# Kernel tuning notes

Measured on AMD Instinct MI355X. Metric: run time of the kernel, lower is better.

Reference implementation:

```python
import jax, jax.numpy as jnp
import numpy as np

B, S, D, DFF = 4, 2048, 1024, 4096
EPS = 1e-5


def layernorm(x, gamma, beta):
    mu = jnp.mean(x, axis=-1, keepdims=True)
    var = jnp.var(x, axis=-1, keepdims=True)
    return (x - mu) * jax.lax.rsqrt(var + EPS) * gamma + beta


def attention(Q, K, V, causal):
    d_k = Q.shape[-1]
    scores = jnp.einsum('bqd,bkd->bqk', Q, K) / jnp.sqrt(jnp.asarray(d_k, Q.dtype))
    if causal:
        q_len, k_len = scores.shape[-2], scores.shape[-1]
        mask = jnp.tril(jnp.ones((q_len, k_len), dtype=bool))
        scores = jnp.where(mask[None], scores, jnp.asarray(-jnp.inf, scores.dtype))
    w = jax.nn.softmax(scores, axis=-1)
    return jnp.einsum('bqk,bkd->bqd', w, V)


def setup_inputs() -> dict:
    key = jax.random.key(0)
    ks = jax.random.split(key, 12)
    sd = 0.02
    return {
        'y': jax.random.normal(ks[0], (B, S, D), jnp.float32),
        'Z': jax.random.normal(ks[1], (B, S, D), jnp.float32),
        'w1': jax.random.normal(ks[2], (D, DFF), jnp.float32) * sd,
        'b1': jnp.zeros((DFF,), jnp.float32),
        'w2': jax.random.normal(ks[3], (DFF, D), jnp.float32) * sd,
        'b2': jnp.zeros((D,), jnp.float32),
        'g1': jnp.ones((D,), jnp.float32), 'beta1': jnp.zeros((D,), jnp.float32),
        'g2': jnp.ones((D,), jnp.float32), 'beta2': jnp.zeros((D,), jnp.float32),
        'g3': jnp.ones((D,), jnp.float32), 'beta3': jnp.zeros((D,), jnp.float32),
    }


def reference(y, Z, w1, b1, w2, b2, g1, beta1, g2, beta2, g3, beta3):
    # masked (causal) self-attention, single head over full d_model
    sa = attention(y, y, y, causal=True)
    y = layernorm(y + sa, g1, beta1)
    # cross-attention to encoder memory Z
    ca = attention(y, Z, Z, causal=False)
    y = layernorm(y + ca, g2, beta2)
    # position-wise FFN
    h = jax.nn.relu(jnp.einsum('bsd,df->bsf', y, w1) + b1)
    ff = jnp.einsum('bsf,fd->bsd', h, w2) + b2
    y = layernorm(y + ff, g3, beta3)
    return y
```

## Files before the change

### kernel.cpp

```cpp
#include <hip/hip_runtime.h>
#include <hip/hip_bf16.h>
#include <hip/hip_fp8.h>


#define Bb 4
#define Ss 2048
#define Dd 1024
#define Ff 4096

typedef __attribute__((ext_vector_type(4))) float f32x4;
typedef __attribute__((ext_vector_type(8))) short bf16x8;
typedef __attribute__((ext_vector_type(2))) long i64x2;
typedef __attribute__((ext_vector_type(8))) unsigned short u16x8;
typedef __attribute__((ext_vector_type(4))) unsigned short u16x4;

__device__ __forceinline__ unsigned short f2bf(float f) {
  unsigned u = __float_as_uint(f);
  u += 0x7FFFu + ((u >> 16) & 1u);
  return (unsigned short)(u >> 16);
}
__device__ __forceinline__ float bf2f(unsigned short h) {
  return __uint_as_float(((unsigned)h) << 16);
}
__device__ __forceinline__ unsigned char f2f8(float f) {
  __hip_fp8_e4m3 q(f);
  return q.__x;
}
__device__ __forceinline__ int f8col(int c) {
  int g = c >> 6, b = c & 63, o = b >> 3, j = b & 7;
  return g * 64 + (2 * (o & 3) + (o >> 2)) * 8 + j;
}

__device__ __forceinline__ void gload_lds16(const void* g, void* l) {
  __builtin_amdgcn_global_load_lds((const __attribute__((address_space(1))) void*)g,
                                   (__attribute__((address_space(3))) void*)l, 16, 0, 0);
}

__device__ __forceinline__ int xcd8(int orig, int n) {
  int q = n >> 3, r = n & 7;
  int x = orig & 7;
  int base = x < r ? x * (q + 1) : r * (q + 1) + (x - r) * q;
  return base + (orig >> 3);
}

__global__ __launch_bounds__(256) void k_transpose_cast(const float* __restrict__ in,
                                                        unsigned short* __restrict__ outT,
                                                        unsigned char* __restrict__ out8,
                                                        int R, int C) {
  __shared__ float t[32][33];
  size_t bo = (size_t)blockIdx.z * R * C;
  const float* pin = in + bo;
  unsigned short* poutT = outT + bo;
  unsigned char* pout8 = out8 ? out8 + bo : nullptr;
  int c0 = blockIdx.x * 32, r0 = blockIdx.y * 32;
  int tx = threadIdx.x, ty = threadIdx.y;
#pragma unroll
  for (int i = 0; i < 4; i++) {
    float v = pin[(size_t)(r0 + ty + i * 8) * C + c0 + tx];
    t[ty + i * 8][tx] = v;
    if (pout8) pout8[(size_t)(r0 + ty + i * 8) * C + f8col(c0 + tx)] = f2f8(v);
  }
  __syncthreads();
#pragma unroll
  for (int i = 0; i < 4; i++)
    poutT[(size_t)(c0 + ty + i * 8) * R + r0 + tx] = f2bf(t[tx][ty + i * 8]);
}

#define BAR() __builtin_amdgcn_s_barrier()
#define PRIO1() __builtin_amdgcn_s_setprio(1)
#define PRIO0() __builtin_amdgcn_s_setprio(0)

#define LDA8(arr, mh, bo)                                                       \
  {                                                                             \
    _Pragma("unroll") for (int j_ = 0; j_ < QM; ++j_) {                         \
      _Pragma("unroll") for (int kh_ = 0; kh_ < 2; ++kh_) {                     \
        arr[j_][kh_] =                                                          \
            *(const bf16x8*)(lds + (bo) + ((mh)*QM + j_) * 2048 + aof[kh_]);    \
      }                                                                         \
    }                                                                           \
  }

#define LDB8(arr, nh, bo)                                                       \
  {                                                                             \
    _Pragma("unroll") for (int n_ = 0; n_ < 2; ++n_) {                          \
      _Pragma("unroll") for (int kh_ = 0; kh_ < 2; ++kh_) {                     \
        arr[n_][kh_] =                                                          \
            *(const bf16x8*)(lds + (bo) + ((nh)*2 + n_) * 2048 + bof[kh_]);     \
      }                                                                         \
    }                                                                           \
  }

#define MMQ(aarr, barr, mh, nh)                                                 \
  {                                                                             \
    _Pragma("unroll") for (int j_ = 0; j_ < QM; ++j_) {                         \
      _Pragma("unroll") for (int n_ = 0; n_ < 2; ++n_) {                        \
        _Pragma("unroll") for (int kh_ = 0; kh_ < 2; ++kh_) {                   \
          acc[(mh)*QM + j_][(nh)*2 + n_] = __builtin_amdgcn_mfma_f32_16x16x32_bf16( \
              aarr[j_][kh_], barr[n_][kh_], acc[(mh)*QM + j_][(nh)*2 + n_], 0, 0, 0); \
        }                                                                       \
      }                                                                         \
    }                                                                           \
  }

#define LDAF8(arr, mh, bo)                                                      \
  {                                                                             \
    _Pragma("unroll") for (int j_ = 0; j_ < 4; ++j_)                            \
        arr[j_] = *(const i64x2*)(lds + (bo) + ((mh)*4 + j_) * 1024 + aofs);    \
  }
#define LDBF8(arr, nh, bo)                                                      \
  {                                                                             \
    _Pragma("unroll") for (int n_ = 0; n_ < 2; ++n_)                            \
        arr[n_] = *(const i64x2*)(lds + (bo) + ((nh)*2 + n_) * 1024 + bofs);    \
  }
#define MMQF8(aarr, barr, mh, nh)                                               \
  {                                                                             \
    _Pragma("unroll") for (int j_ = 0; j_ < 4; ++j_) {                          \
      _Pragma("unroll") for (int n_ = 0; n_ < 2; ++n_) {                        \
        _Pragma("unroll") for (int kh_ = 0; kh_ < 2; ++kh_) {                   \
          acc[(mh)*4 + j_][(nh)*2 + n_] = __builtin_amdgcn_mfma_f32_16x16x32_fp8_fp8( \
              aarr[j_][kh_], barr[n_][kh_], acc[(mh)*4 + j_][(nh)*2 + n_], 0, 0, 0);  \
        }                                                                       \
      }                                                                         \
    }                                                                           \
  }

#define EPILOGUE(MR_, WMS_)                                                     \
  {                                                                             \
    const int colb = j0 + wc * 64 + fr;                                         \
    const int rowb = i0 + wr * (WMS_) + (kq << 2);                              \
    const size_t cb = (size_t)bz * bsC;                                         \
    _Pragma("unroll") for (int m = 0; m < (MR_); ++m) {                         \
      _Pragma("unroll") for (int r = 0; r < 4; ++r) {                           \
        size_t ro = cb + (size_t)(rowb + m * 16 + r) * ldc;                     \
        _Pragma("unroll") for (int n = 0; n < 4; ++n) {                         \
          float v = acc[m][n][r];                                               \
          int col = colb + n * 16;                                              \
          if (EPI == 0) Cb[ro + col] = f2bf(v * scale);                         \
          else if (EPI == 2) Cb[ro + col] = f2bf(fmaxf(v + bias[col], 0.f));    \
          else if (EPI == 4) Cb[ro + col] = f2bf(v + residF[ro + col]);         \
          else if (EPI == 6) Cb[ro + col] = f2bf(v + bf2f(residB[ro + col]));   \
          else Cb[ro + col] = f2bf(v + bias[col] + bf2f(residB[ro + col]));     \
        }                                                                       \
      }                                                                         \
    }                                                                           \
  }

template <bool CAUSAL>
__global__ __launch_bounds__(512) void k_gemm8f8(
    const unsigned char* __restrict__ Ag, const unsigned char* __restrict__ Bg,
    unsigned short* __restrict__ Cb,
    int K, int lda, int ldb, int ldc, long bsA, long bsB, long bsC, float scale) {
  constexpr int ABYTES = 16384, BBYTES = 16384;
  __shared__ alignas(16) char lds[2 * ABYTES + 2 * BBYTES];

  int i0, j0;
  if (CAUSAL) {
    int t = xcd8(blockIdx.x, gridDim.x);
    int ti = (int)((sqrtf(8.f * t + 1.f) - 1.f) * 0.5f);
    while ((ti + 1) * (ti + 2) / 2 <= t) ++ti;
    while (ti * (ti + 1) / 2 > t) --ti;
    i0 = ti * 256;
    j0 = (t - ti * (ti + 1) / 2) * 256;
  } else {
    int lin = xcd8(blockIdx.y * gridDim.x + blockIdx.x, gridDim.x * gridDim.y);
    i0 = (lin / gridDim.x) * 256;
    j0 = (lin % gridDim.x) * 256;
  }
  int bz = blockIdx.z;
  Ag += (size_t)bz * bsA;
  Bg += (size_t)bz * bsB;

  const int nk = K / 64;
  const int niter = nk / 2;

  const int tid = threadIdx.x;
  const int w = tid >> 6, lane = tid & 63;
  const int wr = w >> 2, wc = w & 3;

  const int srow = tid >> 2;
  const int scs = (tid & 3) ^ ((tid >> 3) & 3);
  const unsigned char* As = Ag + (size_t)(i0 + srow) * lda + scs * 16;
  const unsigned char* Bs = Bg + (size_t)(j0 + srow) * ldb + scs * 16;

  auto stA = [&](int kt, int hf) {
    int ks = kt < nk ? kt : nk - 1;
    gload_lds16(As + (size_t)(hf * 128) * lda + ks * 64,
                lds + (kt & 1) * ABYTES + hf * 8192 + w * 1024);
  };
  auto stB = [&](int kt, int hf) {
    int ks = kt < nk ? kt : nk - 1;
    gload_lds16(Bs + (size_t)(hf * 128) * ldb + ks * 64,
                lds + 2 * ABYTES + (kt & 1) * BBYTES + hf * 8192 + w * 1024);
  };

  const int fr = lane & 15, kq = lane >> 4;
  const int rA = wr * 128 + fr;
  const int rB = wc * 64 + fr;
  const unsigned aofs = rA * 64 + ((kq ^ ((rA >> 1) & 3)) << 4);
  const unsigned bofs = rB * 64 + ((kq ^ ((rB >> 1) & 3)) << 4);
  constexpr int A0 = 0, A1 = ABYTES, B0 = 2 * ABYTES, B1 = 2 * ABYTES + BBYTES;

  f32x4 acc[8][4];
#pragma unroll
  for (int m = 0; m < 8; ++m)
#pragma unroll
    for (int n = 0; n < 4; ++n) acc[m][n] = (f32x4){0.f, 0.f, 0.f, 0.f};

  i64x2 a0[4], a1[4], b0[2], b1[2];

  stA(0, 0); stA(0, 1); stB(0, 0); stB(0, 1);
  stA(1, 0); stA(1, 1); stB(1, 0);
  asm volatile("s_waitcnt vmcnt(3)" ::: "memory");
  BAR();
  LDAF8(a0, 0, A0); LDBF8(b0, 0, B0);

  for (int t = 0; t < niter; ++t) {
    const int ka = 2 * t + 2, kb = 2 * t + 3;
    LDAF8(a1, 1, A0);
    stB(2 * t + 1, 1);
    BAR(); PRIO1(); MMQF8(a0, b0, 0, 0); PRIO0(); BAR();
    LDBF8(b1, 1, B0);
    stA(ka, 0);
    BAR(); PRIO1(); MMQF8(a1, b0, 1, 0); PRIO0(); BAR();
    stA(ka, 1);
    BAR(); PRIO1(); MMQF8(a0, b1, 0, 1); PRIO0(); BAR();
    stB(ka, 0);
    asm volatile("s_waitcnt vmcnt(3)" ::: "memory");
    BAR();
    LDAF8(a0, 0, A1); LDBF8(b0, 0, B1);
    PRIO1(); MMQF8(a1, b1, 1, 1); PRIO0(); BAR();
    LDAF8(a1, 1, A1);
    stB(ka, 1);
    BAR(); PRIO1(); MMQF8(a0, b0, 0, 0); PRIO0(); BAR();
    LDBF8(b1, 1, B1);
    stA(kb, 0);
    BAR(); PRIO1(); MMQF8(a1, b0, 1, 0); PRIO0(); BAR();
    stA(kb, 1);
    BAR(); PRIO1(); MMQF8(a0, b1, 0, 1); PRIO0(); BAR();
    stB(kb, 0);
    asm volatile("s_waitcnt vmcnt(3)" ::: "memory");
    BAR();
    LDAF8(a0, 0, A0); LDBF8(b0, 0, B0);
    PRIO1(); MMQF8(a1, b1, 1, 1); PRIO0(); BAR();
  }

  const int colb = j0 + wc * 64 + fr;
  const int rowb = i0 + wr * 128 + (kq << 2);
  const size_t cb = (size_t)bz * bsC;
#pragma unroll
  for (int m = 0; m < 8; ++m) {
#pragma unroll
    for (int r = 0; r < 4; ++r) {
      size_t ro = cb + (size_t)(rowb + m * 16 + r) * ldc;
#pragma unroll
      for (int n = 0; n < 4; ++n)
        Cb[ro + colb + n * 16] = f2bf(acc[m][n][r] * scale);
    }
  }
}

template <int EPI, bool CAUSAL>
__global__ __launch_bounds__(512) void k_gemm8(
    const unsigned short* __restrict__ Ag, const unsigned short* __restrict__ Bg,
    unsigned short* __restrict__ Cb,
    const float* __restrict__ bias, const float* __restrict__ residF,
    const unsigned short* __restrict__ residB,
    int K, int lda, int ldb, int ldc, long bsA, long bsB, long bsC, float scale) {
  constexpr int QM = 4;
  constexpr int ABYTES = 32768, BBYTES = 32768;
  __shared__ alignas(16) char lds[2 * ABYTES + 2 * BBYTES];

  int i0, j0;
  if (CAUSAL) {
    int t = xcd8(blockIdx.x, gridDim.x);
    int ti = (int)((sqrtf(8.f * t + 1.f) - 1.f) * 0.5f);
    while ((ti + 1) * (ti + 2) / 2 <= t) ++ti;
    while (ti * (ti + 1) / 2 > t) --ti;
    i0 = ti * 256;
    j0 = (t - ti * (ti + 1) / 2) * 256;
  } else {
    int lin = xcd8(blockIdx.y * gridDim.x + blockIdx.x, gridDim.x * gridDim.y);
    i0 = (lin / gridDim.x) * 256;
    j0 = (lin % gridDim.x) * 256;
  }
  int bz = blockIdx.z;
  Ag += (size_t)bz * bsA;
  Bg += (size_t)bz * bsB;

  const int nk = K / 64;
  const int niter = nk / 2;

  const int tid = threadIdx.x;
  const int w = tid >> 6, lane = tid & 63;
  const int wr = w >> 2, wc = w & 3;

  const int srow = (w << 3) + (lane >> 3);
  const int bcs = (lane & 7) ^ (lane >> 3);
  const unsigned short* As = Ag + (size_t)(i0 + srow) * lda + bcs * 8;
  const unsigned short* Bs = Bg + (size_t)(j0 + srow) * ldb + bcs * 8;
  char* ldsAw = lds + w * 1024;
  char* ldsBw = lds + 2 * ABYTES + w * 1024;

  auto stA = [&](int kt, int hf) {
    int ks = kt < nk ? kt : nk - 1;
#pragma unroll
    for (int l = 0; l < 2; ++l)
      gload_lds16(As + (size_t)(hf * 128 + l * 64) * lda + ks * 64,
                  ldsAw + (kt & 1) * ABYTES + hf * 128 * 128 + l * 8192);
  };
  auto stB = [&](int kt, int hf) {
    int ks = kt < nk ? kt : nk - 1;
#pragma unroll
    for (int l = 0; l < 2; ++l)
      gload_lds16(Bs + (size_t)(hf * 128 + l * 64) * ldb + ks * 64,
                  ldsBw + (kt & 1) * BBYTES + hf * 128 * 128 + l * 8192);
  };

  const int fr = lane & 15, kq = lane >> 4;
  const int rA = wr * 128 + fr;
  const int rB = wc * 64 + fr;
  unsigned aof[2], bof[2];
  aof[0] = rA * 128 + ((kq ^ (rA & 7)) << 4);
  aof[1] = rA * 128 + (((kq + 4) ^ (rA & 7)) << 4);
  bof[0] = 2 * ABYTES + rB * 128 + ((kq ^ (rB & 7)) << 4);
  bof[1] = 2 * ABYTES + rB * 128 + (((kq + 4) ^ (rB & 7)) << 4);
  constexpr int A0 = 0, A1 = ABYTES, B0 = 0, B1 = BBYTES;

  f32x4 acc[8][4];
#pragma unroll
  for (int m = 0; m < 8; ++m)
#pragma unroll
    for (int n = 0; n < 4; ++n) acc[m][n] = (f32x4){0.f, 0.f, 0.f, 0.f};

  bf16x8 a0[QM][2], a1[QM][2], b0[2][2], b1[2][2];

  stA(0, 0); stA(0, 1); stB(0, 0); stB(0, 1);
  stA(1, 0); stA(1, 1); stB(1, 0);
  asm volatile("s_waitcnt vmcnt(6)" ::: "memory");
  BAR();
  LDA8(a0, 0, A0); LDB8(b0, 0, B0);

  for (int t = 0; t < niter; ++t) {
    const int ka = 2 * t + 2, kb = 2 * t + 3;
    LDA8(a1, 1, A0);
    stB(2 * t + 1, 1);
    BAR(); PRIO1(); MMQ(a0, b0, 0, 0); PRIO0(); BAR();
    LDB8(b1, 1, B0);
    stA(ka, 0);
    BAR(); PRIO1(); MMQ(a1, b0, 1, 0); PRIO0(); BAR();
    stA(ka, 1);
    BAR(); PRIO1(); MMQ(a0, b1, 0, 1); PRIO0(); BAR();
    stB(ka, 0);
    asm volatile("s_waitcnt vmcnt(6)" ::: "memory");
    BAR();
    LDA8(a0, 0, A1); LDB8(b0, 0, B1);
    PRIO1(); MMQ(a1, b1, 1, 1); PRIO0(); BAR();
    LDA8(a1, 1, A1);
    stB(ka, 1);
    BAR(); PRIO1(); MMQ(a0, b0, 0, 0); PRIO0(); BAR();
    LDB8(b1, 1, B1);
    stA(kb, 0);
    BAR(); PRIO1(); MMQ(a1, b0, 1, 0); PRIO0(); BAR();
    stA(kb, 1);
    BAR(); PRIO1(); MMQ(a0, b1, 0, 1); PRIO0(); BAR();
    stB(kb, 0);
    asm volatile("s_waitcnt vmcnt(6)" ::: "memory");
    BAR();
    LDA8(a0, 0, A0); LDB8(b0, 0, B0);
    PRIO1(); MMQ(a1, b1, 1, 1); PRIO0(); BAR();
  }
  EPILOGUE(8, 128)
}

template <int EPI, bool KCAP>
__global__ __launch_bounds__(512) void k_gemm4(
    const unsigned short* __restrict__ Ag, const unsigned short* __restrict__ Bg,
    unsigned short* __restrict__ Cb,
    const float* __restrict__ bias, const float* __restrict__ residF,
    const unsigned short* __restrict__ residB,
    int K, int lda, int ldb, int ldc, long bsA, long bsB, long bsC, float scale) {
  constexpr int QM = 4;
  constexpr int ABYTES = 16384, BBYTES = 32768;
  __shared__ alignas(16) char lds[2 * ABYTES + 2 * BBYTES];

  int lin = xcd8(blockIdx.y * gridDim.x + blockIdx.x, gridDim.x * gridDim.y);
  int i0 = (lin / gridDim.x) * 128;
  int j0 = (lin % gridDim.x) * 256;
  int bz = blockIdx.z;
  Ag += (size_t)bz * bsA;
  Bg += (size_t)bz * bsB;

  int nk = K / 64;
  if (KCAP) {
    int cap = i0 / 64 + 2;
    nk = nk < cap ? nk : cap;
  }
  const int niter = nk / 2;

  const int tid = threadIdx.x;
  const int w = tid >> 6, lane = tid & 63;
  const int wr = w >> 2, wc = w & 3;

  const int srow = (w << 3) + (lane >> 3);
  const int bcs = (lane & 7) ^ (lane >> 3);
  const unsigned short* As = Ag + (size_t)(i0 + srow) * lda + bcs * 8;
  const unsigned short* Bs = Bg + (size_t)(j0 + srow) * ldb + bcs * 8;
  char* ldsAw = lds + w * 1024;
  char* ldsBw = lds + 2 * ABYTES + w * 1024;

  auto stA2 = [&](int kt) {
    int ks = kt < nk ? kt : nk - 1;
#pragma unroll
    for (int hf = 0; hf < 2; ++hf)
      gload_lds16(As + (size_t)(hf * 64) * lda + ks * 64,
                  ldsAw + (kt & 1) * ABYTES + hf * 64 * 128);
  };
  auto stBh = [&](int kt, int hf) {
    int ks = kt < nk ? kt : nk - 1;
#pragma unroll
    for (int l = 0; l < 2; ++l)
      gload_lds16(Bs + (size_t)(hf * 128 + l * 64) * ldb + ks * 64,
                  ldsBw + (kt & 1) * BBYTES + hf * 128 * 128 + l * 8192);
  };

  const int fr = lane & 15, kq = lane >> 4;
  const int rA = wr * 64 + fr;
  const int rB = wc * 64 + fr;
  unsigned aof[2], bof[2];
  aof[0] = rA * 128 + ((kq ^ (rA & 7)) << 4);
  aof[1] = rA * 128 + (((kq + 4) ^ (rA & 7)) << 4);
  bof[0] = 2 * ABYTES + rB * 128 + ((kq ^ (rB & 7)) << 4);
  bof[1] = 2 * ABYTES + rB * 128 + (((kq + 4) ^ (rB & 7)) << 4);
  constexpr int A0 = 0, A1 = ABYTES, B0 = 0, B1 = BBYTES;

  f32x4 acc[4][4];
#pragma unroll
  for (int m = 0; m < 4; ++m)
#pragma unroll
    for (int n = 0; n < 4; ++n) acc[m][n] = (f32x4){0.f, 0.f, 0.f, 0.f};

  bf16x8 a[QM][2], b0[2][2], b1[2][2];

  stA2(0); stBh(0, 0); stBh(0, 1);
  stA2(1); stBh(1, 0);
  asm volatile("s_waitcnt vmcnt(4)" ::: "memory");
  BAR();
  LDA8(a, 0, A0); LDB8(b0, 0, B0);

  for (int t = 0; t < niter; ++t) {
    const int ka = 2 * t + 2, kb = 2 * t + 3;
    LDB8(b1, 1, B0);
    stBh(2 * t + 1, 1);
    BAR(); PRIO1(); MMQ(a, b0, 0, 0); PRIO0(); BAR();
    stA2(ka); stBh(ka, 0);
    asm volatile("s_waitcnt vmcnt(4)" ::: "memory");
    BAR();
    PRIO1(); MMQ(a, b1, 0, 1); PRIO0();
    LDA8(a, 0, A1); LDB8(b0, 0, B1);
    BAR();
    LDB8(b1, 1, B1);
    stBh(ka, 1);
    BAR(); PRIO1(); MMQ(a, b0, 0, 0); PRIO0(); BAR();
    stA2(kb); stBh(kb, 0);
    asm volatile("s_waitcnt vmcnt(4)" ::: "memory");
    BAR();
    PRIO1(); MMQ(a, b1, 0, 1); PRIO0();
    LDA8(a, 0, A0); LDB8(b0, 0, B0);
    BAR();
  }
  EPILOGUE(4, 64)
}

template <bool CAUSAL>
__global__ __launch_bounds__(256) void k_softmax(unsigned short* __restrict__ scores) {
  int row = blockIdx.x;
  int i = row & (Ss - 1);
  unsigned short* src = scores + (size_t)row * Ss;
  int nv = CAUSAL ? i + 1 : Ss;
  int nb = CAUSAL ? ((i & ~127) + 128) : Ss;
  int t = threadIdx.x;
  int w = t >> 6, lane = t & 63;
  bool act = t * 8 < nb;
  float v[8];
  float mx = -1e30f;
  if (act) {
    u16x8 raw = *(const u16x8*)(src + t * 8);
#pragma unroll
    for (int k = 0; k < 8; k++) {
      int j = t * 8 + k;
      v[k] = (j < nv) ? bf2f(raw[k]) : -1e30f;
      mx = fmaxf(mx, v[k]);
    }
  } else {
#pragma unroll
    for (int k = 0; k < 8; k++) v[k] = -1e30f;
  }
#pragma unroll
  for (int o = 32; o; o >>= 1) mx = fmaxf(mx, __shfl_xor(mx, o));
  __shared__ float red[8];
  if (lane == 0) red[w] = mx;
  __syncthreads();
  mx = fmaxf(fmaxf(red[0], red[1]), fmaxf(red[2], red[3]));
  float sum = 0.f;
#pragma unroll
  for (int k = 0; k < 8; k++) {
    float e = (v[k] > -1e29f) ? __expf(v[k] - mx) : 0.f;
    v[k] = e;
    sum += e;
  }
#pragma unroll
  for (int o = 32; o; o >>= 1) sum += __shfl_xor(sum, o);
  if (lane == 0) red[4 + w] = sum;
  __syncthreads();
  sum = red[4] + red[5] + red[6] + red[7];
  float inv = 1.f / sum;
  if (act) {
    u16x8 r;
#pragma unroll
    for (int k = 0; k < 8; k++) r[k] = f2bf(v[k] * inv);
    *(u16x8*)(src + t * 8) = r;
  }
}

template <int OM>
__global__ __launch_bounds__(256) void k_ln(const unsigned short* __restrict__ a,
                                            const float* __restrict__ g,
                                            const float* __restrict__ be,
                                            float* __restrict__ outf,
                                            unsigned short* __restrict__ outb,
                                            unsigned char* __restrict__ out8) {
  int row = blockIdx.x;
  size_t o = (size_t)row * Dd;
  int t = threadIdx.x;
  u16x4 raw = *(const u16x4*)(a + o + t * 4);
  f32x4 x;
#pragma unroll
  for (int k = 0; k < 4; k++) x[k] = bf2f(raw[k]);
  float s = x[0] + x[1] + x[2] + x[3];
  float q = x[0] * x[0] + x[1] * x[1] + x[2] * x[2] + x[3] * x[3];
  int w = t >> 6, lane = t & 63;
#pragma unroll
  for (int of = 32; of; of >>= 1) {
    s += __shfl_xor(s, of);
    q += __shfl_xor(q, of);
  }
  __shared__ float red[8];
  if (lane == 0) {
    red[w] = s;
    red[4 + w] = q;
  }
  __syncthreads();
  s = red[0] + red[1] + red[2] + red[3];
  q = red[4] + red[5] + red[6] + red[7];
  float mean = s * (1.f / Dd);
  float var = q * (1.f / Dd) - mean * mean;
  float rstd = rsqrtf(var + 1e-5f);
  f32x4 gv = *(const f32x4*)(g + t * 4);
  f32x4 bv = *(const f32x4*)(be + t * 4);
  f32x4 y;
#pragma unroll
  for (int k = 0; k < 4; k++) y[k] = (x[k] - mean) * rstd * gv[k] + bv[k];
  if (OM == 0) {
    *(f32x4*)(outf + o + t * 4) = y;
  } else {
    u16x4 r;
    r[0] = f2bf(y[0]); r[1] = f2bf(y[1]); r[2] = f2bf(y[2]); r[3] = f2bf(y[3]);
    *(u16x4*)(outb + o + t * 4) = r;
    if (OM == 2) {
      int cbyte = t * 4;
      int gq = cbyte >> 6, oo = (cbyte >> 3) & 7, j = cbyte & 7;
      int phys = gq * 64 + (2 * (oo & 3) + (oo >> 2)) * 8 + j;
      unsigned rr = (unsigned)f2f8(y[0]) | ((unsigned)f2f8(y[1]) << 8) |
                    ((unsigned)f2f8(y[2]) << 16) | ((unsigned)f2f8(y[3]) << 24);
      *(unsigned*)(out8 + (size_t)row * Dd + phys) = rr;
    }
  }
}

extern "C" void kernel_launch(void* const* d_in, const int* in_sizes, int n_in, void* d_out,
                              int out_size, void* d_ws, size_t ws_size, hipStream_t stream) {
  (void)in_sizes; (void)n_in; (void)out_size; (void)ws_size;
  const float* y   = (const float*)d_in[0];
  const float* Z   = (const float*)d_in[1];
  const float* w1  = (const float*)d_in[2];
  const float* b1  = (const float*)d_in[3];
  const float* w2  = (const float*)d_in[4];
  const float* b2  = (const float*)d_in[5];
  const float* g1  = (const float*)d_in[6];
  const float* be1 = (const float*)d_in[7];
  const float* g2  = (const float*)d_in[8];
  const float* be2 = (const float*)d_in[9];
  const float* g3  = (const float*)d_in[10];
  const float* be3 = (const float*)d_in[11];
  float* out = (float*)d_out;

  char* ws = (char*)d_ws;
  const size_t MB = 1024ull * 1024ull;
  unsigned short* T   = (unsigned short*)(ws);
  unsigned short* y1b = (unsigned short*)(ws);
  unsigned short* ffo = (unsigned short*)(ws);
  unsigned short* Zt  = (unsigned short*)(ws + 16 * MB);
  unsigned short* ybf = (unsigned short*)(ws + 32 * MB);
  unsigned short* w1t = (unsigned short*)(ws + 48 * MB);
  unsigned short* w2t = (unsigned short*)(ws + 56 * MB);
  unsigned short* sc  = (unsigned short*)(ws + 64 * MB);
  unsigned short* h   = (unsigned short*)(ws + 64 * MB);
  unsigned char* y8   = (unsigned char*)(ws + 96 * MB);
  unsigned char* Z8   = (unsigned char*)(ws + 104 * MB);
  unsigned char* y18  = (unsigned char*)(ws + 112 * MB);
  unsigned short* attnb = (unsigned short*)d_out;

  dim3 b256(256), b512(512);
  const float scl = 1.f / 32.f;
  const long SD = (long)Ss * Dd, SS = (long)Ss * Ss;

  k_transpose_cast<<<dim3(Dd / 32, Ss / 32, Bb), dim3(32, 8), 0, stream>>>(y, T, y8, Ss, Dd);
  k_transpose_cast<<<dim3(Dd / 32, Ss / 32, Bb), dim3(32, 8), 0, stream>>>(Z, Zt, Z8, Ss, Dd);
  k_transpose_cast<<<dim3(Ff / 32, Dd / 32, 1), dim3(32, 8), 0, stream>>>(w1, w1t, nullptr, Dd, Ff);
  k_transpose_cast<<<dim3(Dd / 32, Ff / 32, 1), dim3(32, 8), 0, stream>>>(w2, w2t, nullptr, Ff, Dd);

  k_gemm8f8<true><<<dim3(36, 1, Bb), b512, 0, stream>>>(
      y8, y8, sc, Dd, Dd, Dd, Ss, SD, SD, SS, scl);
  k_softmax<true><<<dim3(Bb * Ss), b256, 0, stream>>>(sc);
  k_gemm4<4, true><<<dim3(Dd / 256, Ss / 128, Bb), b512, 0, stream>>>(
      sc, T, attnb, nullptr, y, nullptr, Ss, Ss, Ss, Dd, SS, SD, SD, 1.f);
  k_ln<2><<<dim3(Bb * Ss), b256, 0, stream>>>(attnb, g1, be1, nullptr, y1b, y18);

  k_gemm8f8<false><<<dim3(Ss / 256, Ss / 256, Bb), b512, 0, stream>>>(
      y18, Z8, sc, Dd, Dd, Dd, Ss, SD, SD, SS, scl);
  k_softmax<false><<<dim3(Bb * Ss), b256, 0, stream>>>(sc);
  k_gemm4<6, false><<<dim3(Dd / 256, Ss / 128, Bb), b512, 0, stream>>>(
      sc, Zt, attnb, nullptr, nullptr, y1b, Ss, Ss, Ss, Dd, SS, SD, SD, 1.f);
  k_ln<1><<<dim3(Bb * Ss), b256, 0, stream>>>(attnb, g2, be2, nullptr, ybf, nullptr);

  k_gemm8<2, false><<<dim3(Ff / 256, (Bb * Ss) / 256, 1), b512, 0, stream>>>(
      ybf, w1t, h, b1, nullptr, nullptr, Dd, Dd, Dd, Ff, 0L, 0L, 0L, 1.f);
  k_gemm4<7, false><<<dim3(Dd / 256, (Bb * Ss) / 128, 1), b512, 0, stream>>>(
      h, w2t, ffo, b2, nullptr, ybf, Ff, Ff, Ff, Dd, 0L, 0L, 0L, 1.f);
  k_ln<0><<<dim3(Bb * Ss), b256, 0, stream>>>(ffo, g3, be3, out, nullptr, nullptr);
}
```

Before: 353.5 us.

## Split causal PV GEMM over K into two halves, sum partials in layernorm

Replaces the causal P·V GEMM with a dedicated kernel that splits each row-tile's causal K range into two balanced halves run by separate blocks. Each half writes a bf16 partial, the first including the fp32 residual, and the following layernorm adds the two partials. This doubles the grid and evens out the triangular work so the GPU is better filled. It also merges the y and Z transpose/cast launches into one. The cost is an extra bf16 partial buffer written and read, plus partial sums rounded to bf16 before they are added.

```diff
diff --git a/kernel.cpp b/kernel.cpp
--- a/kernel.cpp
+++ b/kernel.cpp
@@ -43,23 +43,46 @@
   return base + (orig >> 3);
 }
 
-__global__ __launch_bounds__(256) void k_transpose_cast(const float* __restrict__ in,
-                                                        unsigned short* __restrict__ outT,
-                                                        unsigned char* __restrict__ out8,
-                                                        int R, int C) {
+__global__ __launch_bounds__(256) void k_transpose2(const float* __restrict__ inA,
+                                                    const float* __restrict__ inB,
+                                                    unsigned short* __restrict__ outTA,
+                                                    unsigned short* __restrict__ outTB,
+                                                    unsigned char* __restrict__ out8A,
+                                                    unsigned char* __restrict__ out8B,
+                                                    int R, int C) {
   __shared__ float t[32][33];
-  size_t bo = (size_t)blockIdx.z * R * C;
-  const float* pin = in + bo;
-  unsigned short* poutT = outT + bo;
-  unsigned char* pout8 = out8 ? out8 + bo : nullptr;
+  int z = blockIdx.z;
+  bool second = z >= Bb;
+  int b = second ? z - Bb : z;
+  size_t bo = (size_t)b * R * C;
+  const float* pin = (second ? inB : inA) + bo;
+  unsigned short* poutT = (second ? outTB : outTA) + bo;
+  unsigned char* pout8 = (second ? out8B : out8A) + bo;
   int c0 = blockIdx.x * 32, r0 = blockIdx.y * 32;
   int tx = threadIdx.x, ty = threadIdx.y;
 #pragma unroll
   for (int i = 0; i < 4; i++) {
     float v = pin[(size_t)(r0 + ty + i * 8) * C + c0 + tx];
     t[ty + i * 8][tx] = v;
-    if (pout8) pout8[(size_t)(r0 + ty + i * 8) * C + f8col(c0 + tx)] = f2f8(v);
-  }
+    pout8[(size_t)(r0 + ty + i * 8) * C + f8col(c0 + tx)] = f2f8(v);
+  }
+  __syncthreads();
+#pragma unroll
+  for (int i = 0; i < 4; i++)
+    poutT[(size_t)(c0 + ty + i * 8) * R + r0 + tx] = f2bf(t[tx][ty + i * 8]);
+}
+
+__global__ __launch_bounds__(256) void k_transpose_cast(const float* __restrict__ in,
+                                                        unsigned short* __restrict__ outT,
+                                                        int R, int C) {
+  __shared__ float t[32][33];
+  const float* pin = in;
+  unsigned short* poutT = outT;
+  int c0 = blockIdx.x * 32, r0 = blockIdx.y * 32;
+  int tx = threadIdx.x, ty = threadIdx.y;
+#pragma unroll
+  for (int i = 0; i < 4; i++)
+    t[ty + i * 8][tx] = pin[(size_t)(r0 + ty + i * 8) * C + c0 + tx];
   __syncthreads();
 #pragma unroll
   for (int i = 0; i < 4; i++)
@@ -137,7 +160,6 @@
           int col = colb + n * 16;                                              \
           if (EPI == 0) Cb[ro + col] = f2bf(v * scale);                         \
           else if (EPI == 2) Cb[ro + col] = f2bf(fmaxf(v + bias[col], 0.f));    \
-          else if (EPI == 4) Cb[ro + col] = f2bf(v + residF[ro + col]);         \
           else if (EPI == 6) Cb[ro + col] = f2bf(v + bf2f(residB[ro + col]));   \
           else Cb[ro + col] = f2bf(v + bias[col] + bf2f(residB[ro + col]));     \
         }                                                                       \
@@ -263,8 +285,7 @@
 __global__ __launch_bounds__(512) void k_gemm8(
     const unsigned short* __restrict__ Ag, const unsigned short* __restrict__ Bg,
     unsigned short* __restrict__ Cb,
-    const float* __restrict__ bias, const float* __restrict__ residF,
-    const unsigned short* __restrict__ residB,
+    const float* __restrict__ bias, const unsigned short* __restrict__ residB,
     int K, int lda, int ldb, int ldc, long bsA, long bsB, long bsC, float scale) {
   constexpr int QM = 4;
   constexpr int ABYTES = 32768, BBYTES = 32768;
@@ -376,8 +397,7 @@
 __global__ __launch_bounds__(512) void k_gemm4(
     const unsigned short* __restrict__ Ag, const unsigned short* __restrict__ Bg,
     unsigned short* __restrict__ Cb,
-    const float* __restrict__ bias, const float* __restrict__ residF,
-    const unsigned short* __restrict__ residB,
+    const float* __restrict__ bias, const unsigned short* __restrict__ residB,
     int K, int lda, int ldb, int ldc, long bsA, long bsB, long bsC, float scale) {
   constexpr int QM = 4;
   constexpr int ABYTES = 16384, BBYTES = 32768;
@@ -469,6 +489,120 @@
     BAR();
   }
   EPILOGUE(4, 64)
+}
+
+__global__ __launch_bounds__(512) void k_pv1(
+    const unsigned short* __restrict__ Ag, const unsigned short* __restrict__ Bg,
+    unsigned short* __restrict__ C0, unsigned short* __restrict__ C1,
+    const float* __restrict__ residF) {
+  constexpr int QM = 4;
+  constexpr int ABYTES = 16384, BBYTES = 32768;
+  __shared__ alignas(16) char lds[2 * ABYTES + 2 * BBYTES];
+  const int lda = Ss, ldb = Ss, ldc = Dd;
+
+  const int xc = blockIdx.x & 3, kh = blockIdx.x >> 2;
+  const int iy = blockIdx.y;
+  const int i0 = iy * 128, j0 = xc * 256;
+  const int bz = blockIdx.z;
+  Ag += (size_t)bz * ((long)Ss * Ss);
+  Bg += (size_t)bz * ((long)Dd * Ss);
+
+  const int cap = 2 * iy + 2;
+  const int nA = (iy + 2) & ~1;
+  const int kbase = kh ? nA : 0;
+  const int nkr = kh ? cap - nA : nA;
+  const int niter = nkr / 2;
+
+  const int tid = threadIdx.x;
+  const int w = tid >> 6, lane = tid & 63;
+  const int wr = w >> 2, wc = w & 3;
+
+  const int srow = (w << 3) + (lane >> 3);
+  const int bcs = (lane & 7) ^ (lane >> 3);
+  const unsigned short* As = Ag + (size_t)(i0 + srow) * lda + bcs * 8;
+  const unsigned short* Bs = Bg + (size_t)(j0 + srow) * ldb + bcs * 8;
+  char* ldsAw = lds + w * 1024;
+  char* ldsBw = lds + 2 * ABYTES + w * 1024;
+
+  auto stA2 = [&](int kt) {
+    int ks = kbase + (kt < nkr ? kt : (nkr > 0 ? nkr - 1 : 0));
+#pragma unroll
+    for (int hf = 0; hf < 2; ++hf)
+      gload_lds16(As + (size_t)(hf * 64) * lda + ks * 64,
+                  ldsAw + (kt & 1) * ABYTES + hf * 64 * 128);
+  };
+  auto stBh = [&](int kt, int hf) {
+    int ks = kbase + (kt < nkr ? kt : (nkr > 0 ? nkr - 1 : 0));
+#pragma unroll
+    for (int l = 0; l < 2; ++l)
+      gload_lds16(Bs + (size_t)(hf * 128 + l * 64) * ldb + ks * 64,
+                  ldsBw + (kt & 1) * BBYTES + hf * 128 * 128 + l * 8192);
+  };
+
+  const int fr = lane & 15, kq = lane >> 4;
+  const int rA = wr * 64 + fr;
+  const int rB = wc * 64 + fr;
+  unsigned aof[2], bof[2];
+  aof[0] = rA * 128 + ((kq ^ (rA & 7)) << 4);
+  aof[1] = rA * 128 + (((kq + 4) ^ (rA & 7)) << 4);
+  bof[0] = 2 * ABYTES + rB * 128 + ((kq ^ (rB & 7)) << 4);
+  bof[1] = 2 * ABYTES + rB * 128 + (((kq + 4) ^ (rB & 7)) << 4);
+  constexpr int A0 = 0, A1 = ABYTES, B0 = 0, B1 = BBYTES;
+
+  f32x4 acc[4][4];
+#pragma unroll
+  for (int m = 0; m < 4; ++m)
+#pragma unroll
+    for (int n = 0; n < 4; ++n) acc[m][n] = (f32x4){0.f, 0.f, 0.f, 0.f};
+
+  bf16x8 a[QM][2], b0[2][2], b1[2][2];
+
+  stA2(0); stBh(0, 0); stBh(0, 1);
+  stA2(1); stBh(1, 0);
+  asm volatile("s_waitcnt vmcnt(4)" ::: "memory");
+  BAR();
+  LDA8(a, 0, A0); LDB8(b0, 0, B0);
+
+  for (int t = 0; t < niter; ++t) {
+    const int ka = 2 * t + 2, kb = 2 * t + 3;
+    LDB8(b1, 1, B0);
+    stBh(2 * t + 1, 1);
+    BAR(); PRIO1(); MMQ(a, b0, 0, 0); PRIO0(); BAR();
+    stA2(ka); stBh(ka, 0);
+    asm volatile("s_waitcnt vmcnt(4)" ::: "memory");
+    BAR();
+    PRIO1(); MMQ(a, b1, 0, 1); PRIO0();
+    LDA8(a, 0, A1); LDB8(b0, 0, B1);
+    BAR();
+    LDB8(b1, 1, B1);
+    stBh(ka, 1);
+    BAR(); PRIO1(); MMQ(a, b0, 0, 0); PRIO0(); BAR();
+    stA2(kb); stBh(kb, 0);
+    asm volatile("s_waitcnt vmcnt(4)" ::: "memory");
+    BAR();
+    PRIO1(); MMQ(a, b1, 0, 1); PRIO0();
+    LDA8(a, 0, A0); LDB8(b0, 0, B0);
+    BAR();
+  }
+
+  const int colb = j0 + wc * 64 + fr;
+  const int rowb = i0 + wr * 64 + (kq << 2);
+  const size_t cb = (size_t)bz * ((long)Ss * Dd);
+  unsigned short* Cb = kh ? C1 : C0;
+#pragma unroll
+  for (int m = 0; m < 4; ++m) {
+#pragma unroll
+    for (int r = 0; r < 4; ++r) {
+      size_t ro = cb + (size_t)(rowb + m * 16 + r) * ldc;
+#pragma unroll
+      for (int n = 0; n < 4; ++n) {
+        float v = acc[m][n][r];
+        int col = colb + n * 16;
+        if (kh == 0) Cb[ro + col] = f2bf(v + residF[ro + col]);
+        else Cb[ro + col] = f2bf(v);
+      }
+    }
+  }
 }
 
 template <bool CAUSAL>
@@ -524,6 +658,7 @@
 
 template <int OM>
 __global__ __launch_bounds__(256) void k_ln(const unsigned short* __restrict__ a,
+                                            const unsigned short* __restrict__ a2,
                                             const float* __restrict__ g,
                                             const float* __restrict__ be,
                                             float* __restrict__ outf,
@@ -536,6 +671,11 @@
   f32x4 x;
 #pragma unroll
   for (int k = 0; k < 4; k++) x[k] = bf2f(raw[k]);
+  if (a2) {
+    u16x4 raw2 = *(const u16x4*)(a2 + o + t * 4);
+#pragma unroll
+    for (int k = 0; k < 4; k++) x[k] += bf2f(raw2[k]);
+  }
   float s = x[0] + x[1] + x[2] + x[3];
   float q = x[0] * x[0] + x[1] * x[1] + x[2] * x[2] + x[3] * x[3];
   int w = t >> 6, lane = t & 63;
@@ -608,34 +748,34 @@
   unsigned char* y8   = (unsigned char*)(ws + 96 * MB);
   unsigned char* Z8   = (unsigned char*)(ws + 104 * MB);
   unsigned char* y18  = (unsigned char*)(ws + 112 * MB);
-  unsigned short* attnb = (unsigned short*)d_out;
+  unsigned short* attnb  = (unsigned short*)d_out;
+  unsigned short* attnb2 = (unsigned short*)((char*)d_out + 16 * MB);
 
   dim3 b256(256), b512(512);
   const float scl = 1.f / 32.f;
   const long SD = (long)Ss * Dd, SS = (long)Ss * Ss;
 
-  k_transpose_cast<<<dim3(Dd / 32, Ss / 32, Bb), dim3(32, 8), 0, stream>>>(y, T, y8, Ss, Dd);
-  k_transpose_cast<<<dim3(Dd / 32, Ss / 32, Bb), dim3(32, 8), 0, stream>>>(Z, Zt, Z8, Ss, Dd);
-  k_transpose_cast<<<dim3(Ff / 32, Dd / 32, 1), dim3(32, 8), 0, stream>>>(w1, w1t, nullptr, Dd, Ff);
-  k_transpose_cast<<<dim3(Dd / 32, Ff / 32, 1), dim3(32, 8), 0, stream>>>(w2, w2t, nullptr, Ff, Dd);
+  k_transpose2<<<dim3(Dd / 32, Ss / 32, 2 * Bb), dim3(32, 8), 0, stream>>>(
+      y, Z, T, Zt, y8, Z8, Ss, Dd);
+  k_transpose_cast<<<dim3(Ff / 32, Dd / 32, 1), dim3(32, 8), 0, stream>>>(w1, w1t, Dd, Ff);
+  k_transpose_cast<<<dim3(Dd / 32, Ff / 32, 1), dim3(32, 8), 0, stream>>>(w2, w2t, Ff, Dd);
 
   k_gemm8f8<true><<<dim3(36, 1, Bb), b512, 0, stream>>>(
       y8, y8, sc, Dd, Dd, Dd, Ss, SD, SD, SS, scl);
   k_softmax<true><<<dim3(Bb * Ss), b256, 0, stream>>>(sc);
-  k_gemm4<4, true><<<dim3(Dd / 256, Ss / 128, Bb), b512, 0, stream>>>(
-      sc, T, attnb, nullptr, y, nullptr, Ss, Ss, Ss, Dd, SS, SD, SD, 1.f);
-  k_ln<2><<<dim3(Bb * Ss), b256, 0, stream>>>(attnb, g1, be1, nullptr, y1b, y18);
+  k_pv1<<<dim3(8, Ss / 128, Bb), b512, 0, stream>>>(sc, T, attnb, attnb2, y);
+  k_ln<2><<<dim3(Bb * Ss), b256, 0, stream>>>(attnb, attnb2, g1, be1, nullptr, y1b, y18);
 
   k_gemm8f8<false><<<dim3(Ss / 256, Ss / 256, Bb), b512, 0, stream>>>(
       y18, Z8, sc, Dd, Dd, Dd, Ss, SD, SD, SS, scl);
   k_softmax<false><<<dim3(Bb * Ss), b256, 0, stream>>>(sc);
   k_gemm4<6, false><<<dim3(Dd / 256, Ss / 128, Bb), b512, 0, stream>>>(
-      sc, Zt, attnb, nullptr, nullptr, y1b, Ss, Ss, Ss, Dd, SS, SD, SD, 1.f);
-  k_ln<1><<<dim3(Bb * Ss), b256, 0, stream>>>(attnb, g2, be2, nullptr, ybf, nullptr);
+      sc, Zt, attnb, nullptr, y1b, Ss, Ss, Ss, Dd, SS, SD, SD, 1.f);
+  k_ln<1><<<dim3(Bb * Ss), b256, 0, stream>>>(attnb, nullptr, g2, be2, nullptr, ybf, nullptr);
 
   k_gemm8<2, false><<<dim3(Ff / 256, (Bb * Ss) / 256, 1), b512, 0, stream>>>(
-      ybf, w1t, h, b1, nullptr, nullptr, Dd, Dd, Dd, Ff, 0L, 0L, 0L, 1.f);
+      ybf, w1t, h, b1, nullptr, Dd, Dd, Dd, Ff, 0L, 0L, 0L, 1.f);
   k_gemm4<7, false><<<dim3(Dd / 256, (Bb * Ss) / 128, 1), b512, 0, stream>>>(
-      h, w2t, ffo, b2, nullptr, ybf, Ff, Ff, Ff, Dd, 0L, 0L, 0L, 1.f);
-  k_ln<0><<<dim3(Bb * Ss), b256, 0, stream>>>(ffo, g3, be3, out, nullptr, nullptr);
-}
+      h, w2t, ffo, b2, ybf, Ff, Ff, Ff, Dd, 0L, 0L, 0L, 1.f);
+  k_ln<0><<<dim3(Bb * Ss), b256, 0, stream>>>(ffo, nullptr, g3, be3, out, nullptr, nullptr);
+}
```

After: 374.1 us. +5.8%, slower.
